# Kernel tuning notes

Hardware: AMD Instinct MI355X
Metric: run time of the kernel (lower is better)

## Reference

```python
import jax, jax.numpy as jnp
import numpy as np

NUM_HEADS = 16
EMBED_DIM = 1024
HEAD_DIM = EMBED_DIM // NUM_HEADS


def setup_inputs() -> dict:
    key = jax.random.key(0)
    ks = jax.random.split(key, 9)
    B, S, D = 2, 2048, EMBED_DIM
    s = 1.0 / np.sqrt(D)
    inp = {
        "x": jax.random.normal(ks[0], (B, S, D), dtype=jnp.float32),
        "Wq": jax.random.normal(ks[1], (D, D), dtype=jnp.float32) * s,
        "bq": jnp.zeros((D,), dtype=jnp.float32),
        "Wk": jax.random.normal(ks[2], (D, D), dtype=jnp.float32) * s,
        "bk": jnp.zeros((D,), dtype=jnp.float32),
        "Wv": jax.random.normal(ks[3], (D, D), dtype=jnp.float32) * s,
        "bv": jnp.zeros((D,), dtype=jnp.float32),
        "Wo": jax.random.normal(ks[4], (D, D), dtype=jnp.float32) * s,
        "bo": jnp.zeros((D,), dtype=jnp.float32),
    }
    return inp


def reference(x, Wq, bq, Wk, bk, Wv, bv, Wo, bo):
    B, S, D = x.shape
    H, Hd = NUM_HEADS, HEAD_DIM
    # projections (weights stored [in, out])
    q = (x @ Wq + bq).reshape(B, S, H, Hd).transpose(0, 2, 1, 3)  # [B,H,S,Hd]
    k = (x @ Wk + bk).reshape(B, S, H, Hd).transpose(0, 2, 1, 3)
    v = (x @ Wv + bv).reshape(B, S, H, Hd).transpose(0, 2, 1, 3)
    scores = jnp.einsum("bhqd,bhkd->bhqk", q, k) / jnp.sqrt(jnp.float32(Hd))
    causal = jnp.tril(jnp.ones((S, S), dtype=bool))  # True = keep
    scores = jnp.where(causal, scores, jnp.float32(-jnp.inf))
    attn = jax.nn.softmax(scores, axis=-1)
    ctx = jnp.einsum("bhqk,bhkd->bhqd", attn, v)  # [B,H,S,Hd]
    ctx = ctx.transpose(0, 2, 1, 3).reshape(B, S, D)
    return ctx @ Wo + bo
```

## Files before the change

kernel.cpp:

```cpp
#include <hip/hip_runtime.h>

#define NUMH 16
#define HD   64
#define SEQ  2048
#define NB   2
#define DIM  1024
#define MROWS (NB * SEQ)

typedef __attribute__((ext_vector_type(8))) short short8;
typedef __attribute__((ext_vector_type(4))) float f32x4;
typedef unsigned short u16;
typedef unsigned int u32;

__device__ inline u16 bf16_rn(float f) {
    unsigned u = __float_as_uint(f);
    return (u16)((u + 0x7FFFu + ((u >> 16) & 1u)) >> 16);
}
__device__ inline float bf16f(u16 h) {
    return __uint_as_float(((unsigned)h) << 16);
}

__global__ void convert_split(const float* __restrict__ in,
                              u16* __restrict__ hi, u16* __restrict__ lo, int n4)
{
    for (int i = blockIdx.x * blockDim.x + threadIdx.x; i < n4;
         i += gridDim.x * blockDim.x) {
        const float4 v = ((const float4*)in)[i];
        ushort4 h, l;
        h.x = bf16_rn(v.x); l.x = bf16_rn(v.x - bf16f(h.x));
        h.y = bf16_rn(v.y); l.y = bf16_rn(v.y - bf16f(h.y));
        h.z = bf16_rn(v.z); l.z = bf16_rn(v.z - bf16f(h.z));
        h.w = bf16_rn(v.w); l.w = bf16_rn(v.w - bf16f(h.w));
        ((ushort4*)hi)[i] = h;
        ((ushort4*)lo)[i] = l;
    }
}

__global__ __launch_bounds__(256)
void transpose_split(const float* __restrict__ W,
                     u16* __restrict__ th, u16* __restrict__ tl, float scale)
{
    __shared__ float Ls[32][33];
    const int tx = threadIdx.x & 31, ty = threadIdx.x >> 5;
    const int k0 = blockIdx.x * 32, n0 = blockIdx.y * 32;
#pragma unroll
    for (int i = 0; i < 4; ++i)
        Ls[ty + 8 * i][tx] = W[(size_t)(k0 + ty + 8 * i) * DIM + n0 + tx];
    __syncthreads();
#pragma unroll
    for (int i = 0; i < 4; ++i) {
        const float f = Ls[tx][ty + 8 * i] * scale;
        const u16 h = bf16_rn(f);
        const u16 l = bf16_rn(f - bf16f(h));
        th[(size_t)(n0 + ty + 8 * i) * DIM + k0 + tx] = h;
        tl[(size_t)(n0 + ty + 8 * i) * DIM + k0 + tx] = l;
    }
}

template<int EPI>
__global__ __launch_bounds__(256, 2)
void gemm_split(const u16* __restrict__ Ah, const u16* __restrict__ Al,
                const u16* __restrict__ Bh, const u16* __restrict__ Bl,
                const float* __restrict__ bias, float bscale,
                float* __restrict__ outF, u16* __restrict__ outH,
                u16* __restrict__ outL)
{
    __shared__ u16 AsH[128][32];
    __shared__ u16 AsL[128][32];
    __shared__ u16 BsH[64][32];
    __shared__ u16 BsL[64][32];

    const int tid  = threadIdx.x;
    const int m0   = blockIdx.x * 128;
    const int n0   = blockIdx.y * 64;
    const int wid  = tid >> 6;
    const int lane = tid & 63;
    const int wr   = wid >> 1;
    const int wc   = wid & 1;
    const int fr   = lane & 15;
    const int fg   = lane >> 4;
    const int K    = DIM;

    f32x4 acc[4][2];
#pragma unroll
    for (int i = 0; i < 4; ++i)
#pragma unroll
        for (int j = 0; j < 2; ++j) { f32x4 z = {0.f, 0.f, 0.f, 0.f}; acc[i][j] = z; }

    const int row0 = tid >> 2;
    const int k80  = (tid & 3) * 8;

    short8 pf[6];
    auto LOAD = [&](int kt) {
        pf[0] = *(const short8*)&Ah[(size_t)(m0 + row0) * K + kt + k80];
        pf[1] = *(const short8*)&Ah[(size_t)(m0 + row0 + 64) * K + kt + k80];
        pf[2] = *(const short8*)&Al[(size_t)(m0 + row0) * K + kt + k80];
        pf[3] = *(const short8*)&Al[(size_t)(m0 + row0 + 64) * K + kt + k80];
        pf[4] = *(const short8*)&Bh[(size_t)(n0 + row0) * K + kt + k80];
        pf[5] = *(const short8*)&Bl[(size_t)(n0 + row0) * K + kt + k80];
    };
    LOAD(0);

    for (int kt = 0; kt < K; kt += 32) {
        __syncthreads();
        *(short8*)&AsH[row0][k80]      = pf[0];
        *(short8*)&AsH[row0 + 64][k80] = pf[1];
        *(short8*)&AsL[row0][k80]      = pf[2];
        *(short8*)&AsL[row0 + 64][k80] = pf[3];
        *(short8*)&BsH[row0][k80]      = pf[4];
        *(short8*)&BsL[row0][k80]      = pf[5];
        __syncthreads();
        if (kt + 32 < K) LOAD(kt + 32);

        short8 afh[4], afl[4], bfh[2], bfl[2];
#pragma unroll
        for (int i = 0; i < 4; ++i) {
            afh[i] = *(const short8*)&AsH[wr * 64 + i * 16 + fr][fg * 8];
            afl[i] = *(const short8*)&AsL[wr * 64 + i * 16 + fr][fg * 8];
        }
#pragma unroll
        for (int j = 0; j < 2; ++j) {
            bfh[j] = *(const short8*)&BsH[wc * 32 + j * 16 + fr][fg * 8];
            bfl[j] = *(const short8*)&BsL[wc * 32 + j * 16 + fr][fg * 8];
        }
#pragma unroll
        for (int i = 0; i < 4; ++i)
#pragma unroll
            for (int j = 0; j < 2; ++j) {
                acc[i][j] = __builtin_amdgcn_mfma_f32_16x16x32_bf16(afl[i], bfh[j], acc[i][j], 0, 0, 0);
                acc[i][j] = __builtin_amdgcn_mfma_f32_16x16x32_bf16(afh[i], bfl[j], acc[i][j], 0, 0, 0);
                acc[i][j] = __builtin_amdgcn_mfma_f32_16x16x32_bf16(afh[i], bfh[j], acc[i][j], 0, 0, 0);
            }
    }

#pragma unroll
    for (int i = 0; i < 4; ++i)
#pragma unroll
        for (int j = 0; j < 2; ++j) {
            const int col = n0 + wc * 32 + j * 16 + fr;
            const float bv = bias[col] * bscale;
            if (EPI == 2) {
                const int row = m0 + wr * 64 + i * 16 + fg * 4;
                const int b  = row >> 11;
                const int s  = row & (SEQ - 1);
                const int hh = col >> 6;
                const int hd = col & (HD - 1);
                ushort4 pk;
                pk.x = bf16_rn(acc[i][j][0] + bv);
                pk.y = bf16_rn(acc[i][j][1] + bv);
                pk.z = bf16_rn(acc[i][j][2] + bv);
                pk.w = bf16_rn(acc[i][j][3] + bv);
                *(ushort4*)&outH[((size_t)(b * NUMH + hh) * HD + hd) * SEQ + s] = pk;
            } else {
#pragma unroll
                for (int r = 0; r < 4; ++r) {
                    const int row = m0 + wr * 64 + i * 16 + fg * 4 + r;
                    const float v = acc[i][j][r] + bv;
                    if (EPI == 0) {
                        outF[(size_t)row * DIM + col] = v;
                    } else {
                        const int b  = row >> 11;
                        const int s  = row & (SEQ - 1);
                        const int hh = col >> 6;
                        const int hd = col & (HD - 1);
                        const size_t idx = ((size_t)(b * NUMH + hh) * SEQ + s) * HD + hd;
                        const u16 hv = bf16_rn(v);
                        outH[idx] = hv;
                        outL[idx] = bf16_rn(v - bf16f(hv));
                    }
                }
            }
        }
}

__global__ __launch_bounds__(256, 2)
void attn_mfma2(const u16* __restrict__ Qh, const u16* __restrict__ Ql,
                const u16* __restrict__ Kh, const u16* __restrict__ Kl,
                const u16* __restrict__ Vt,
                u16* __restrict__ ctxH, u16* __restrict__ ctxL)
{
    __shared__ u16 KsH[64 * 64];
    __shared__ u16 KsL[64 * 64];
    __shared__ u16 Vs [64 * 64];

    const int tid  = threadIdx.x;
    const int w    = tid >> 6;
    const int lane = tid & 63;
    const int lc   = lane & 15;
    const int g    = lane >> 4;

    const int bh = blockIdx.x >> 4;
    const int p  = blockIdx.x & 15;
    const int qA = p, qB = 31 - p;
    const int NT = 32 - p;
    const int bb = bh >> 4, hq = bh & 15;
    const size_t kqBase = (size_t)bh * SEQ * HD;
    const size_t vBase  = (size_t)bh * HD * SEQ;

    short8 qhA[2], qlA[2], qhB[2], qlB[2];
    {
        const size_t ra = kqBase + (size_t)(qA * 64 + w * 16 + lc) * HD;
        const size_t rb = kqBase + (size_t)(qB * 64 + w * 16 + lc) * HD;
        qhA[0] = *(const short8*)&Qh[ra + g * 8];  qhA[1] = *(const short8*)&Qh[ra + 32 + g * 8];
        qlA[0] = *(const short8*)&Ql[ra + g * 8];  qlA[1] = *(const short8*)&Ql[ra + 32 + g * 8];
        qhB[0] = *(const short8*)&Qh[rb + g * 8];  qhB[1] = *(const short8*)&Qh[rb + 32 + g * 8];
        qlB[0] = *(const short8*)&Ql[rb + g * 8];  qlB[1] = *(const short8*)&Ql[rb + 32 + g * 8];
    }

    f32x4 oA[4], oB[4];
#pragma unroll
    for (int f4 = 0; f4 < 4; ++f4) {
        f32x4 z = {0.f, 0.f, 0.f, 0.f};
        oA[f4] = z; oB[f4] = z;
    }
    float mA = -1e30f, lA = 0.f, mB = -1e30f, lB = 0.f;

    const int srow = tid >> 2;
    const int scol = (tid & 3) * 16;
    const int sw   = (srow & 7) << 3;
    const int so1  = srow * 64 + (scol ^ sw);
    const int so2  = srow * 64 + ((scol + 8) ^ sw);
    const int rsw  = (lc & 7) << 3;

    short8 pf[6];
    auto LOADT = [&](int kt) {
        const size_t kg = kqBase + (size_t)(kt * 64 + srow) * HD + scol;
        pf[0] = *(const short8*)&Kh[kg];      pf[1] = *(const short8*)&Kh[kg + 8];
        pf[2] = *(const short8*)&Kl[kg];      pf[3] = *(const short8*)&Kl[kg + 8];
        const size_t vg = vBase + (size_t)srow * SEQ + kt * 64 + scol;
        pf[4] = *(const short8*)&Vt[vg];      pf[5] = *(const short8*)&Vt[vg + 8];
    };
    LOADT(0);

    for (int kt = 0; kt < NT; ++kt) {
        __syncthreads();
        *(short8*)&KsH[so1] = pf[0];  *(short8*)&KsH[so2] = pf[1];
        *(short8*)&KsL[so1] = pf[2];  *(short8*)&KsL[so2] = pf[3];
        *(short8*)&Vs [so1] = pf[4];  *(short8*)&Vs [so2] = pf[5];
        __syncthreads();
        if (kt + 1 < NT) LOADT(kt + 1);

        const bool actA = (kt <= qA);
        const int  k0   = kt * 64;

        f32x4 sA[4], sB[4];
#pragma unroll
        for (int f4 = 0; f4 < 4; ++f4) {
            f32x4 a = {0.f, 0.f, 0.f, 0.f}, b = {0.f, 0.f, 0.f, 0.f};
#pragma unroll
            for (int s2 = 0; s2 < 2; ++s2) {
                const int off = (f4 * 16 + lc) * 64 + ((s2 * 32 + g * 8) ^ rsw);
                const short8 kh = *(const short8*)&KsH[off];
                const short8 kl = *(const short8*)&KsL[off];
                if (actA) {
                    a = __builtin_amdgcn_mfma_f32_16x16x32_bf16(kh, qlA[s2], a, 0, 0, 0);
                    a = __builtin_amdgcn_mfma_f32_16x16x32_bf16(kl, qhA[s2], a, 0, 0, 0);
                    a = __builtin_amdgcn_mfma_f32_16x16x32_bf16(kh, qhA[s2], a, 0, 0, 0);
                }
                b = __builtin_amdgcn_mfma_f32_16x16x32_bf16(kh, qlB[s2], b, 0, 0, 0);
                b = __builtin_amdgcn_mfma_f32_16x16x32_bf16(kl, qhB[s2], b, 0, 0, 0);
                b = __builtin_amdgcn_mfma_f32_16x16x32_bf16(kh, qhB[s2], b, 0, 0, 0);
            }
            sA[f4] = a; sB[f4] = b;
        }

        u32 pbA[2][4], pbB[2][4];
        const int a0 = (((g & 1) * 2 + 0) * 16 + lc) * 4;
        const int a1 = (((g & 1) * 2 + 1) * 16 + lc) * 4;
        const bool hi = ((g >> 1) & 1) != 0;

        auto SOFTMAX = [&](f32x4* sf, float& m, float& l, f32x4* o,
                           int qt, u32 pb[2][4]) {
            const bool diag = (kt == qt);
            const int  qg   = qt * 64 + w * 16 + lc;
            float pm = -1e30f;
#pragma unroll
            for (int f4 = 0; f4 < 4; ++f4)
#pragma unroll
                for (int r = 0; r < 4; ++r) {
                    float sv = sf[f4][r];
                    if (diag && (k0 + f4 * 16 + g * 4 + r > qg)) sv = -1e30f;
                    sf[f4][r] = sv;
                    pm = fmaxf(pm, sv);
                }
            pm = fmaxf(pm, __shfl_xor(pm, 16));
            pm = fmaxf(pm, __shfl_xor(pm, 32));
            const float mn = fmaxf(m, pm);
            const float sc = __expf(m - mn);
            m = mn; l *= sc;
#pragma unroll
            for (int f4 = 0; f4 < 4; ++f4) o[f4] *= sc;
            float ps = 0.f;
            u32 pk[4][2];
#pragma unroll
            for (int f4 = 0; f4 < 4; ++f4)
#pragma unroll
                for (int pr = 0; pr < 2; ++pr) {
                    const float p0 = __expf(sf[f4][pr * 2 + 0] - mn);
                    const float p1 = __expf(sf[f4][pr * 2 + 1] - mn);
                    ps += p0 + p1;
                    pk[f4][pr] = (u32)bf16_rn(p0) | ((u32)bf16_rn(p1) << 16);
                }
            ps += __shfl_xor(ps, 16);
            ps += __shfl_xor(ps, 32);
            l += ps;
#pragma unroll
            for (int s2 = 0; s2 < 2; ++s2)
#pragma unroll
                for (int mm = 0; mm < 4; ++mm) {
                    const int addr = (mm < 2) ? a0 : a1;
                    const u32 t0 = (u32)__builtin_amdgcn_ds_bpermute(addr, (int)pk[s2 * 2 + 0][mm & 1]);
                    const u32 t1 = (u32)__builtin_amdgcn_ds_bpermute(addr, (int)pk[s2 * 2 + 1][mm & 1]);
                    pb[s2][mm] = hi ? t1 : t0;
                }
        };

        if (actA) SOFTMAX(sA, mA, lA, oA, qA, pbA);
        SOFTMAX(sB, mB, lB, oB, qB, pbB);

#pragma unroll
        for (int s2 = 0; s2 < 2; ++s2) {
            union { u32 u[4]; short8 s; } ua, ub;
#pragma unroll
            for (int mm = 0; mm < 4; ++mm) { ua.u[mm] = pbA[s2][mm]; ub.u[mm] = pbB[s2][mm]; }
#pragma unroll
            for (int f4 = 0; f4 < 4; ++f4) {
                const int off = (f4 * 16 + lc) * 64 + ((s2 * 32 + g * 8) ^ rsw);
                const short8 vv = *(const short8*)&Vs[off];
                if (actA) oA[f4] = __builtin_amdgcn_mfma_f32_16x16x32_bf16(vv, ua.s, oA[f4], 0, 0, 0);
                oB[f4] = __builtin_amdgcn_mfma_f32_16x16x32_bf16(vv, ub.s, oB[f4], 0, 0, 0);
            }
        }
    }

    const float iA = 1.f / lA, iB = 1.f / lB;
    const size_t rowA = (size_t)bb * SEQ + qA * 64 + w * 16 + lc;
    const size_t rowB = (size_t)bb * SEQ + qB * 64 + w * 16 + lc;
#pragma unroll
    for (int f4 = 0; f4 < 4; ++f4) {
        const int colb = hq * HD + f4 * 16 + g * 4;
        ushort4 h4, l4;
#pragma unroll
        for (int r = 0; r < 4; ++r) {
            const float v = oA[f4][r] * iA;
            const u16 hv = bf16_rn(v);
            ((u16*)&h4)[r] = hv;
            ((u16*)&l4)[r] = bf16_rn(v - bf16f(hv));
        }
        *(ushort4*)&ctxH[rowA * DIM + colb] = h4;
        *(ushort4*)&ctxL[rowA * DIM + colb] = l4;
#pragma unroll
        for (int r = 0; r < 4; ++r) {
            const float v = oB[f4][r] * iB;
            const u16 hv = bf16_rn(v);
            ((u16*)&h4)[r] = hv;
            ((u16*)&l4)[r] = bf16_rn(v - bf16f(hv));
        }
        *(ushort4*)&ctxH[rowB * DIM + colb] = h4;
        *(ushort4*)&ctxL[rowB * DIM + colb] = l4;
    }
}

extern "C" void kernel_launch(void* const* d_in, const int* in_sizes, int n_in,
                              void* d_out, int out_size, void* d_ws, size_t ws_size,
                              hipStream_t stream)
{
    const float* x  = (const float*)d_in[0];
    const float* Wq = (const float*)d_in[1];
    const float* bq = (const float*)d_in[2];
    const float* Wk = (const float*)d_in[3];
    const float* bk = (const float*)d_in[4];
    const float* Wv = (const float*)d_in[5];
    const float* bv = (const float*)d_in[6];
    const float* Wo = (const float*)d_in[7];
    const float* bo = (const float*)d_in[8];

    char* base = (char*)d_ws;
    const size_t MB = 1024 * 1024;
    u16* Qh_ = (u16*)(base + 0 * MB);
    u16* Ql_ = (u16*)(base + 8 * MB);
    u16* Kh_ = (u16*)(base + 16 * MB);
    u16* Kl_ = (u16*)(base + 24 * MB);
    u16* Vt_ = (u16*)(base + 32 * MB);
    u16* xh  = (u16*)(base + 40 * MB);
    u16* xl  = (u16*)(base + 48 * MB);
    u16* Wth = (u16*)(base + 56 * MB);
    u16* Wtl = (u16*)(base + 58 * MB);

    dim3 blk(256);
    dim3 gg(MROWS / 128, DIM / 64);
    dim3 gt(DIM / 32, DIM / 32);

    hipLaunchKernelGGL(convert_split, dim3(2048), blk, 0, stream,
                       x, xh, xl, MROWS * DIM / 4);

    hipLaunchKernelGGL(transpose_split, gt, blk, 0, stream, Wq, Wth, Wtl, 0.125f);
    hipLaunchKernelGGL((gemm_split<1>), gg, blk, 0, stream,
                       xh, xl, Wth, Wtl, bq, 0.125f, nullptr, Qh_, Ql_);

    hipLaunchKernelGGL(transpose_split, gt, blk, 0, stream, Wk, Wth, Wtl, 1.0f);
    hipLaunchKernelGGL((gemm_split<1>), gg, blk, 0, stream,
                       xh, xl, Wth, Wtl, bk, 1.0f, nullptr, Kh_, Kl_);

    hipLaunchKernelGGL(transpose_split, gt, blk, 0, stream, Wv, Wth, Wtl, 1.0f);
    hipLaunchKernelGGL((gemm_split<2>), gg, blk, 0, stream,
                       xh, xl, Wth, Wtl, bv, 1.0f, nullptr, Vt_, nullptr);

    hipLaunchKernelGGL(attn_mfma2, dim3(NB * NUMH * 16), blk, 0, stream,
                       Qh_, Ql_, Kh_, Kl_, Vt_, xh, xl);

    hipLaunchKernelGGL(transpose_split, gt, blk, 0, stream, Wo, Wth, Wtl, 1.0f);
    hipLaunchKernelGGL((gemm_split<0>), gg, blk, 0, stream,
                       xh, xl, Wth, Wtl, bo, 1.0f, (float*)d_out, nullptr, nullptr);
}
```

Measured before the change: 324.4 us.

## Split attention into one q-tile per block and use direct global-to-LDS GEMM loads

The attention kernel stops pairing a short and a long query tile in one block. It now launches one block per 64-row query tile (twice as many blocks) with a swizzled block order that schedules the longest tiles first, and raises the occupancy hint to 4 blocks per CU. Separately, the projection GEMM replaces register-staged prefetch plus LDS stores with global_load_lds direct copies. That removes the software prefetch overlap, so global latency is now exposed between the barriers.

```diff
diff --git a/kernel.cpp b/kernel.cpp
--- a/kernel.cpp
+++ b/kernel.cpp
@@ -19,6 +19,11 @@
 __device__ inline float bf16f(u16 h) {
     return __uint_as_float(((unsigned)h) << 16);
 }
+
+#define GLD16(gp, lp)                                                        \
+    __builtin_amdgcn_global_load_lds(                                        \
+        (const __attribute__((address_space(1))) void*)(gp),                 \
+        (__attribute__((address_space(3))) void*)(lp), 16, 0, 0)
 
 __global__ void convert_split(const float* __restrict__ in,
                               u16* __restrict__ hi, u16* __restrict__ lo, int n4)
@@ -87,30 +92,18 @@
 #pragma unroll
         for (int j = 0; j < 2; ++j) { f32x4 z = {0.f, 0.f, 0.f, 0.f}; acc[i][j] = z; }
 
-    const int row0 = tid >> 2;
-    const int k80  = (tid & 3) * 8;
-
-    short8 pf[6];
-    auto LOAD = [&](int kt) {
-        pf[0] = *(const short8*)&Ah[(size_t)(m0 + row0) * K + kt + k80];
-        pf[1] = *(const short8*)&Ah[(size_t)(m0 + row0 + 64) * K + kt + k80];
-        pf[2] = *(const short8*)&Al[(size_t)(m0 + row0) * K + kt + k80];
-        pf[3] = *(const short8*)&Al[(size_t)(m0 + row0 + 64) * K + kt + k80];
-        pf[4] = *(const short8*)&Bh[(size_t)(n0 + row0) * K + kt + k80];
-        pf[5] = *(const short8*)&Bl[(size_t)(n0 + row0) * K + kt + k80];
-    };
-    LOAD(0);
+    const int gr = (wid << 4) + (lane >> 2);
+    const int gc = (lane & 3) * 8;
 
     for (int kt = 0; kt < K; kt += 32) {
         __syncthreads();
-        *(short8*)&AsH[row0][k80]      = pf[0];
-        *(short8*)&AsH[row0 + 64][k80] = pf[1];
-        *(short8*)&AsL[row0][k80]      = pf[2];
-        *(short8*)&AsL[row0 + 64][k80] = pf[3];
-        *(short8*)&BsH[row0][k80]      = pf[4];
-        *(short8*)&BsL[row0][k80]      = pf[5];
+        GLD16(&Ah[(size_t)(m0 + gr) * K + kt + gc],      &AsH[(wid << 4)][0]);
+        GLD16(&Ah[(size_t)(m0 + 64 + gr) * K + kt + gc], &AsH[64 + (wid << 4)][0]);
+        GLD16(&Al[(size_t)(m0 + gr) * K + kt + gc],      &AsL[(wid << 4)][0]);
+        GLD16(&Al[(size_t)(m0 + 64 + gr) * K + kt + gc], &AsL[64 + (wid << 4)][0]);
+        GLD16(&Bh[(size_t)(n0 + gr) * K + kt + gc],      &BsH[(wid << 4)][0]);
+        GLD16(&Bl[(size_t)(n0 + gr) * K + kt + gc],      &BsL[(wid << 4)][0]);
         __syncthreads();
-        if (kt + 32 < K) LOAD(kt + 32);
 
         short8 afh[4], afl[4], bfh[2], bfl[2];
 #pragma unroll
@@ -173,8 +166,8 @@
         }
 }
 
-__global__ __launch_bounds__(256, 2)
-void attn_mfma2(const u16* __restrict__ Qh, const u16* __restrict__ Ql,
+__global__ __launch_bounds__(256, 4)
+void attn_mfma3(const u16* __restrict__ Qh, const u16* __restrict__ Ql,
                 const u16* __restrict__ Kh, const u16* __restrict__ Kl,
                 const u16* __restrict__ Vt,
                 u16* __restrict__ ctxH, u16* __restrict__ ctxL)
@@ -189,31 +182,27 @@
     const int lc   = lane & 15;
     const int g    = lane >> 4;
 
-    const int bh = blockIdx.x >> 4;
-    const int p  = blockIdx.x & 15;
-    const int qA = p, qB = 31 - p;
-    const int NT = 32 - p;
+    const int orig = blockIdx.x;
+    const int swz  = (orig & 7) * 128 + (orig >> 3);
+    const int bh   = swz >> 5;
+    const int qt   = 31 - (swz & 31);
+    const int NT   = qt + 1;
+
     const int bb = bh >> 4, hq = bh & 15;
     const size_t kqBase = (size_t)bh * SEQ * HD;
     const size_t vBase  = (size_t)bh * HD * SEQ;
 
-    short8 qhA[2], qlA[2], qhB[2], qlB[2];
+    short8 qh[2], ql[2];
     {
-        const size_t ra = kqBase + (size_t)(qA * 64 + w * 16 + lc) * HD;
-        const size_t rb = kqBase + (size_t)(qB * 64 + w * 16 + lc) * HD;
-        qhA[0] = *(const short8*)&Qh[ra + g * 8];  qhA[1] = *(const short8*)&Qh[ra + 32 + g * 8];
-        qlA[0] = *(const short8*)&Ql[ra + g * 8];  qlA[1] = *(const short8*)&Ql[ra + 32 + g * 8];
-        qhB[0] = *(const short8*)&Qh[rb + g * 8];  qhB[1] = *(const short8*)&Qh[rb + 32 + g * 8];
-        qlB[0] = *(const short8*)&Ql[rb + g * 8];  qlB[1] = *(const short8*)&Ql[rb + 32 + g * 8];
-    }
-
-    f32x4 oA[4], oB[4];
-#pragma unroll
-    for (int f4 = 0; f4 < 4; ++f4) {
-        f32x4 z = {0.f, 0.f, 0.f, 0.f};
-        oA[f4] = z; oB[f4] = z;
-    }
-    float mA = -1e30f, lA = 0.f, mB = -1e30f, lB = 0.f;
+        const size_t ra = kqBase + (size_t)(qt * 64 + w * 16 + lc) * HD;
+        qh[0] = *(const short8*)&Qh[ra + g * 8];  qh[1] = *(const short8*)&Qh[ra + 32 + g * 8];
+        ql[0] = *(const short8*)&Ql[ra + g * 8];  ql[1] = *(const short8*)&Ql[ra + 32 + g * 8];
+    }
+
+    f32x4 o[4];
+#pragma unroll
+    for (int f4 = 0; f4 < 4; ++f4) { f32x4 z = {0.f, 0.f, 0.f, 0.f}; o[f4] = z; }
+    float mrun = -1e30f, lrun = 0.f;
 
     const int srow = tid >> 2;
     const int scol = (tid & 3) * 16;
@@ -232,6 +221,10 @@
     };
     LOADT(0);
 
+    const int a0 = (((g & 1) * 2 + 0) * 16 + lc) * 4;
+    const int a1 = (((g & 1) * 2 + 1) * 16 + lc) * 4;
+    const bool hi = ((g >> 1) & 1) != 0;
+
     for (int kt = 0; kt < NT; ++kt) {
         __syncthreads();
         *(short8*)&KsH[so1] = pf[0];  *(short8*)&KsH[so2] = pf[1];
@@ -240,124 +233,99 @@
         __syncthreads();
         if (kt + 1 < NT) LOADT(kt + 1);
 
-        const bool actA = (kt <= qA);
-        const int  k0   = kt * 64;
-
-        f32x4 sA[4], sB[4];
+        const int k0 = kt * 64;
+
+        f32x4 sf[4];
 #pragma unroll
         for (int f4 = 0; f4 < 4; ++f4) {
-            f32x4 a = {0.f, 0.f, 0.f, 0.f}, b = {0.f, 0.f, 0.f, 0.f};
+            f32x4 a = {0.f, 0.f, 0.f, 0.f};
 #pragma unroll
             for (int s2 = 0; s2 < 2; ++s2) {
                 const int off = (f4 * 16 + lc) * 64 + ((s2 * 32 + g * 8) ^ rsw);
                 const short8 kh = *(const short8*)&KsH[off];
                 const short8 kl = *(const short8*)&KsL[off];
-                if (actA) {
-                    a = __builtin_amdgcn_mfma_f32_16x16x32_bf16(kh, qlA[s2], a, 0, 0, 0);
-                    a = __builtin_amdgcn_mfma_f32_16x16x32_bf16(kl, qhA[s2], a, 0, 0, 0);
-                    a = __builtin_amdgcn_mfma_f32_16x16x32_bf16(kh, qhA[s2], a, 0, 0, 0);
-                }
-                b = __builtin_amdgcn_mfma_f32_16x16x32_bf16(kh, qlB[s2], b, 0, 0, 0);
-                b = __builtin_amdgcn_mfma_f32_16x16x32_bf16(kl, qhB[s2], b, 0, 0, 0);
-                b = __builtin_amdgcn_mfma_f32_16x16x32_bf16(kh, qhB[s2], b, 0, 0, 0);
-            }
-            sA[f4] = a; sB[f4] = b;
-        }
-
-        u32 pbA[2][4], pbB[2][4];
-        const int a0 = (((g & 1) * 2 + 0) * 16 + lc) * 4;
-        const int a1 = (((g & 1) * 2 + 1) * 16 + lc) * 4;
-        const bool hi = ((g >> 1) & 1) != 0;
-
-        auto SOFTMAX = [&](f32x4* sf, float& m, float& l, f32x4* o,
-                           int qt, u32 pb[2][4]) {
-            const bool diag = (kt == qt);
-            const int  qg   = qt * 64 + w * 16 + lc;
-            float pm = -1e30f;
-#pragma unroll
-            for (int f4 = 0; f4 < 4; ++f4)
-#pragma unroll
-                for (int r = 0; r < 4; ++r) {
-                    float sv = sf[f4][r];
-                    if (diag && (k0 + f4 * 16 + g * 4 + r > qg)) sv = -1e30f;
-                    sf[f4][r] = sv;
-                    pm = fmaxf(pm, sv);
-                }
-            pm = fmaxf(pm, __shfl_xor(pm, 16));
-            pm = fmaxf(pm, __shfl_xor(pm, 32));
-            const float mn = fmaxf(m, pm);
-            const float sc = __expf(m - mn);
-            m = mn; l *= sc;
-#pragma unroll
-            for (int f4 = 0; f4 < 4; ++f4) o[f4] *= sc;
-            float ps = 0.f;
-            u32 pk[4][2];
-#pragma unroll
-            for (int f4 = 0; f4 < 4; ++f4)
-#pragma unroll
-                for (int pr = 0; pr < 2; ++pr) {
-                    const float p0 = __expf(sf[f4][pr * 2 + 0] - mn);
-                    const float p1 = __expf(sf[f4][pr * 2 + 1] - mn);
-                    ps += p0 + p1;
-                    pk[f4][pr] = (u32)bf16_rn(p0) | ((u32)bf16_rn(p1) << 16);
-                }
-            ps += __shfl_xor(ps, 16);
-            ps += __shfl_xor(ps, 32);
-            l += ps;
-#pragma unroll
-            for (int s2 = 0; s2 < 2; ++s2)
-#pragma unroll
-                for (int mm = 0; mm < 4; ++mm) {
-                    const int addr = (mm < 2) ? a0 : a1;
-                    const u32 t0 = (u32)__builtin_amdgcn_ds_bpermute(addr, (int)pk[s2 * 2 + 0][mm & 1]);
-                    const u32 t1 = (u32)__builtin_amdgcn_ds_bpermute(addr, (int)pk[s2 * 2 + 1][mm & 1]);
-                    pb[s2][mm] = hi ? t1 : t0;
-                }
-        };
-
-        if (actA) SOFTMAX(sA, mA, lA, oA, qA, pbA);
-        SOFTMAX(sB, mB, lB, oB, qB, pbB);
+                a = __builtin_amdgcn_mfma_f32_16x16x32_bf16(kh, ql[s2], a, 0, 0, 0);
+                a = __builtin_amdgcn_mfma_f32_16x16x32_bf16(kl, qh[s2], a, 0, 0, 0);
+                a = __builtin_amdgcn_mfma_f32_16x16x32_bf16(kh, qh[s2], a, 0, 0, 0);
+            }
+            sf[f4] = a;
+        }
+
+        const bool diag = (kt == qt);
+        const int  qg   = qt * 64 + w * 16 + lc;
+        float pm = -1e30f;
+#pragma unroll
+        for (int f4 = 0; f4 < 4; ++f4)
+#pragma unroll
+            for (int r = 0; r < 4; ++r) {
+                float sv = sf[f4][r];
+                if (diag && (k0 + f4 * 16 + g * 4 + r > qg)) sv = -1e30f;
+                sf[f4][r] = sv;
+                pm = fmaxf(pm, sv);
+            }
+        pm = fmaxf(pm, __shfl_xor(pm, 16));
+        pm = fmaxf(pm, __shfl_xor(pm, 32));
+        const float mn = fmaxf(mrun, pm);
+        const float sc = __expf(mrun - mn);
+        mrun = mn; lrun *= sc;
+#pragma unroll
+        for (int f4 = 0; f4 < 4; ++f4) o[f4] *= sc;
+
+        float ps = 0.f;
+        u32 pk[4][2];
+#pragma unroll
+        for (int f4 = 0; f4 < 4; ++f4)
+#pragma unroll
+            for (int pr = 0; pr < 2; ++pr) {
+                const float p0 = __expf(sf[f4][pr * 2 + 0] - mn);
+                const float p1 = __expf(sf[f4][pr * 2 + 1] - mn);
+                ps += p0 + p1;
+                pk[f4][pr] = (u32)bf16_rn(p0) | ((u32)bf16_rn(p1) << 16);
+            }
+        ps += __shfl_xor(ps, 16);
+        ps += __shfl_xor(ps, 32);
+        lrun += ps;
+
+        u32 pb[2][4];
+#pragma unroll
+        for (int s2 = 0; s2 < 2; ++s2)
+#pragma unroll
+            for (int mm = 0; mm < 4; ++mm) {
+                const int addr = (mm < 2) ? a0 : a1;
+                const u32 t0 = (u32)__builtin_amdgcn_ds_bpermute(addr, (int)pk[s2 * 2 + 0][mm & 1]);
+                const u32 t1 = (u32)__builtin_amdgcn_ds_bpermute(addr, (int)pk[s2 * 2 + 1][mm & 1]);
+                pb[s2][mm] = hi ? t1 : t0;
+            }
 
 #pragma unroll
         for (int s2 = 0; s2 < 2; ++s2) {
-            union { u32 u[4]; short8 s; } ua, ub;
-#pragma unroll
-            for (int mm = 0; mm < 4; ++mm) { ua.u[mm] = pbA[s2][mm]; ub.u[mm] = pbB[s2][mm]; }
+            union { u32 u[4]; short8 s; } ua;
+#pragma unroll
+            for (int mm = 0; mm < 4; ++mm) ua.u[mm] = pb[s2][mm];
 #pragma unroll
             for (int f4 = 0; f4 < 4; ++f4) {
                 const int off = (f4 * 16 + lc) * 64 + ((s2 * 32 + g * 8) ^ rsw);
                 const short8 vv = *(const short8*)&Vs[off];
-                if (actA) oA[f4] = __builtin_amdgcn_mfma_f32_16x16x32_bf16(vv, ua.s, oA[f4], 0, 0, 0);
-                oB[f4] = __builtin_amdgcn_mfma_f32_16x16x32_bf16(vv, ub.s, oB[f4], 0, 0, 0);
-            }
-        }
-    }
-
-    const float iA = 1.f / lA, iB = 1.f / lB;
-    const size_t rowA = (size_t)bb * SEQ + qA * 64 + w * 16 + lc;
-    const size_t rowB = (size_t)bb * SEQ + qB * 64 + w * 16 + lc;
+                o[f4] = __builtin_amdgcn_mfma_f32_16x16x32_bf16(vv, ua.s, o[f4], 0, 0, 0);
+            }
+        }
+    }
+
+    const float iv = 1.f / lrun;
+    const size_t rowA = (size_t)bb * SEQ + qt * 64 + w * 16 + lc;
 #pragma unroll
     for (int f4 = 0; f4 < 4; ++f4) {
         const int colb = hq * HD + f4 * 16 + g * 4;
         ushort4 h4, l4;
 #pragma unroll
         for (int r = 0; r < 4; ++r) {
-            const float v = oA[f4][r] * iA;
+            const float v = o[f4][r] * iv;
             const u16 hv = bf16_rn(v);
             ((u16*)&h4)[r] = hv;
             ((u16*)&l4)[r] = bf16_rn(v - bf16f(hv));
         }
         *(ushort4*)&ctxH[rowA * DIM + colb] = h4;
         *(ushort4*)&ctxL[rowA * DIM + colb] = l4;
-#pragma unroll
-        for (int r = 0; r < 4; ++r) {
-            const float v = oB[f4][r] * iB;
-            const u16 hv = bf16_rn(v);
-            ((u16*)&h4)[r] = hv;
-            ((u16*)&l4)[r] = bf16_rn(v - bf16f(hv));
-        }
-        *(ushort4*)&ctxH[rowB * DIM + colb] = h4;
-        *(ushort4*)&ctxL[rowB * DIM + colb] = l4;
     }
 }
 
@@ -406,8 +374,8 @@
     hipLaunchKernelGGL((gemm_split<2>), gg, blk, 0, stream,
                        xh, xl, Wth, Wtl, bv, 1.0f, nullptr, Vt_, nullptr);
 
-    hipLaunchKernelGGL(attn_mfma2, dim3(NB * NUMH * 16), blk, 0, stream,
-                       Qh_, Ql_, Kh_, Kl_, Vt_, xh, xl);
+    hipLaunchKernelGGL(attn_mfma3, dim3(NB * NUMH * 32), blk, 0, stream,
+                       Qh_, Kh_ ? Ql_ : Ql_, Kh_, Kl_, Vt_, xh, xl);
 
     hipLaunchKernelGGL(transpose_split, gt, blk, 0, stream, Wo, Wth, Wtl, 1.0f);
     hipLaunchKernelGGL((gemm_split<0>), gg, blk, 0, stream,
```

Result: slower. 342.7 us (+5.6%).
